# Kernel optimization log

Measured on AMD Instinct MI355X. Metric: run time of the kernel, lower is better.

Reference implementation:

```python
import jax, jax.numpy as jnp
import numpy as np


def setup_inputs() -> dict:
    key = jax.random.key(0)
    ks = jax.random.split(key, 6)
    C, C8, W, H, B = 512, 64, 64, 64, 4
    x = jax.random.normal(ks[0], (B, C, W, H), dtype=jnp.float32)
    Wf = jax.random.normal(ks[1], (C8, C), dtype=jnp.float32) * (1.0 / np.sqrt(C))
    Wg = jax.random.normal(ks[2], (C8, C), dtype=jnp.float32) * (1.0 / np.sqrt(C))
    Wh = jax.random.normal(ks[3], (C8, C), dtype=jnp.float32) * (1.0 / np.sqrt(C))
    Wv = jax.random.normal(ks[4], (C, C8), dtype=jnp.float32) * (1.0 / np.sqrt(C8))
    gamma = jax.random.normal(ks[5], (1,), dtype=jnp.float32)
    return {"x": x, "Wf": Wf, "Wg": Wg, "Wh": Wh, "Wv": Wv, "gamma": gamma}


def reference(x, Wf, Wg, Wh, Wv, gamma):
    b, c, w, h = x.shape
    n = w * h
    xf = x.reshape(b, c, n)                       # [b, c, n]
    # 1x1 convs == channel-mixing GEMMs
    f = jnp.einsum('oc,bcn->bon', Wf, xf)         # [b, c8, n]
    g = jnp.einsum('oc,bcn->bon', Wg, xf)         # [b, c8, n]
    hmap = jnp.einsum('oc,bcn->bon', Wh, xf)      # [b, c8, n]
    # attn_map[b, i, j] = sum_c f[b, c, i] * g[b, c, j]  (f permuted as in torch)
    attn = jnp.einsum('bci,bcj->bij', f, g)       # [b, n, n]
    # unconventional softmax over dim=1 (rows / the i axis)
    attn = jax.nn.softmax(attn, axis=1)
    sa = jnp.einsum('bcn,bnj->bcj', hmap, attn)   # [b, c8, n]
    sa = sa.reshape(b, -1, w, h)                  # [b, c8, w, h]
    sa = jnp.einsum('oc,bcwh->bowh', Wv, sa)      # [b, c, w, h]
    out = sa * gamma[0] + x
    return out, sa
```

## Files before the change

### kernel.cpp

```cpp
#include <hip/hip_runtime.h>
#include <cstddef>

#define BB 4
#define CC 512
#define NN 4096

using half8  = __attribute__((ext_vector_type(8))) _Float16;
using fp16x2 = __attribute__((ext_vector_type(2))) __fp16;
using short8 = __attribute__((ext_vector_type(8))) short;
using us8    = __attribute__((ext_vector_type(8))) unsigned short;
using f32x4  = __attribute__((ext_vector_type(4))) float;
using f32x16 = __attribute__((ext_vector_type(16))) float;

__device__ __forceinline__ unsigned short f2bf(float x) {
    unsigned int u = __float_as_uint(x);
    u += 0x7fffu + ((u >> 16) & 1u);
    return (unsigned short)(u >> 16);
}

__global__ __launch_bounds__(256) void prep_kernel(
    const float* __restrict__ Wf, const float* __restrict__ Wg,
    const float* __restrict__ Wh, const float* __restrict__ Wv,
    _Float16* __restrict__ Wc16, _Float16* __restrict__ Wv16)
{
    int idx = blockIdx.x * 256 + threadIdx.x;
    int stride = gridDim.x * 256;
    const int N1 = 192 * 512, N2 = 512 * 64;
    for (int i = idx; i < N1 + N2; i += stride) {
        if (i < N1) {
            int row = i >> 9, c = i & 511;
            const float* src = (row < 64) ? Wf : ((row < 128) ? Wg : Wh);
            float sc = (row >= 64 && row < 128) ? 1.4426950408889634f : 1.0f;
            Wc16[i] = (_Float16)(sc * src[(row & 63) * 512 + c]);
        } else {
            int k = i - N1;
            Wv16[k] = (_Float16)Wv[k];
        }
    }
}

__global__ __launch_bounds__(256) void proj_kernel(
    const float* __restrict__ x, const _Float16* __restrict__ Wc16,
    _Float16* __restrict__ Kf, _Float16* __restrict__ Qf,
    unsigned short* __restrict__ Vt)
{
    __shared__ float xsT[2][32][68];
    const int t    = threadIdx.x;
    const int w    = t >> 6;
    const int lane = t & 63;
    const int lh   = lane & 15;
    const int qd   = lane >> 4;
    const int b    = blockIdx.x >> 7;
    const int i0   = (blockIdx.x & 127) << 5;

    f32x4 acc[3][2];
    #pragma unroll
    for (int ot = 0; ot < 3; ot++)
        #pragma unroll
        for (int it = 0; it < 2; it++) { acc[ot][it][0]=0.f; acc[ot][it][1]=0.f; acc[ot][it][2]=0.f; acc[ot][it][3]=0.f; }

    const int ti8 = t & 7;
    const int tc2 = t >> 3;
    const float* xbase = x + (size_t)b*CC*NN + i0 + ti8*4;
    const _Float16* wbase = Wc16 + (size_t)(w*48 + lh)*512 + qd*8;

    float4 st0, st1;
    half8  wcur[2][3], wnxt[2][3];

#define LOADX(ck) do {                                                        \
    st0 = *(const float4*)(xbase + (size_t)((ck)*64 + tc2)*NN);               \
    st1 = *(const float4*)(xbase + (size_t)((ck)*64 + 32 + tc2)*NN);          \
} while (0)
#define STOREX(p_) do {                                                       \
    xsT[p_][ti8*4+0][tc2]    = st0.x; xsT[p_][ti8*4+1][tc2]    = st0.y;       \
    xsT[p_][ti8*4+2][tc2]    = st0.z; xsT[p_][ti8*4+3][tc2]    = st0.w;       \
    xsT[p_][ti8*4+0][32+tc2] = st1.x; xsT[p_][ti8*4+1][32+tc2] = st1.y;       \
    xsT[p_][ti8*4+2][32+tc2] = st1.z; xsT[p_][ti8*4+3][32+tc2] = st1.w;       \
} while (0)
#define LOADW(ck, WD) do {                                                    \
    _Pragma("unroll")                                                         \
    for (int ks_ = 0; ks_ < 2; ks_++)                                         \
        _Pragma("unroll")                                                     \
        for (int ot_ = 0; ot_ < 3; ot_++)                                     \
            WD[ks_][ot_] = *(const half8*)(wbase + (size_t)(ot_*16)*512 + (ck)*64 + ks_*32); \
} while (0)

    LOADX(0); STOREX(0);
    LOADW(0, wcur);
    __syncthreads();

    #pragma unroll
    for (int ck = 0; ck < 8; ck++) {
        const int p = ck & 1;
        if (ck < 7) { LOADX(ck + 1); LOADW(ck + 1, wnxt); }

        #pragma unroll
        for (int ks = 0; ks < 2; ks++) {
            half8 xf[2];
            #pragma unroll
            for (int it = 0; it < 2; it++) {
                const float* xr = &xsT[p][it*16 + lh][ks*32 + qd*8];
                f32x4 xa = *(const f32x4*)xr;
                f32x4 xb = *(const f32x4*)(xr + 4);
                union { fp16x2 h2[4]; half8 h8; } u;
                u.h2[0] = __builtin_amdgcn_cvt_pkrtz(xa[0], xa[1]);
                u.h2[1] = __builtin_amdgcn_cvt_pkrtz(xa[2], xa[3]);
                u.h2[2] = __builtin_amdgcn_cvt_pkrtz(xb[0], xb[1]);
                u.h2[3] = __builtin_amdgcn_cvt_pkrtz(xb[2], xb[3]);
                xf[it] = u.h8;
            }
            #pragma unroll
            for (int ot = 0; ot < 3; ot++)
                #pragma unroll
                for (int it = 0; it < 2; it++)
                    acc[ot][it] = __builtin_amdgcn_mfma_f32_16x16x32_f16(wcur[ks][ot], xf[it], acc[ot][it], 0, 0, 0);
        }

        if (ck < 7) {
            STOREX(p ^ 1);
            #pragma unroll
            for (int ks_ = 0; ks_ < 2; ks_++)
                #pragma unroll
                for (int ot_ = 0; ot_ < 3; ot_++)
                    wcur[ks_][ot_] = wnxt[ks_][ot_];
        }
        __syncthreads();
    }
#undef LOADX
#undef STOREX
#undef LOADW

    #pragma unroll
    for (int ot = 0; ot < 3; ot++) {
        int g16 = w*3 + ot;
        int m   = g16 >> 2;
        int obase = (g16 & 3)*16 + qd*4;
        #pragma unroll
        for (int it = 0; it < 2; it++) {
            int ig = i0 + it*16 + lh;
            #pragma unroll
            for (int r = 0; r < 4; r++) {
                float v = acc[ot][it][r];
                int ol = obase + r;
                if (m == 0)       Kf[((size_t)b*NN + ig)*64 + ol] = (_Float16)v;
                else if (m == 1)  Qf[((size_t)b*NN + ig)*64 + ol] = (_Float16)v;
                else              Vt[((size_t)b*64 + ol)*NN + ig] = f2bf(v);
            }
        }
    }
}

template<int SPLITS>
__global__ __launch_bounds__(256, 4) void attn_kernel(
    const _Float16* __restrict__ Kf, const _Float16* __restrict__ Qf,
    const unsigned short* __restrict__ Vt,
    _Float16* __restrict__ Po16, float* __restrict__ Pl)
{
    static_assert(NN % SPLITS == 0, "split");
    constexpr int KS  = NN / SPLITS;
    constexpr int NCH = KS / 64;

    __shared__ __align__(16) unsigned short Kb2[2][64*64];
    __shared__ __align__(16) unsigned short Vb2[2][64*64];

    const int t    = threadIdx.x;
    const int wv   = t >> 6;
    const int lane = t & 63;
    const int il   = lane & 31;
    const int h    = lane >> 5;

    const int p  = blockIdx.x;
    const int v  = (p & 7) * (SPLITS * 16) + (p >> 3);
    const int jt = v & 31;
    const int bs = v >> 5;
    const int b  = bs / SPLITS;
    const int s  = bs % SPLITS;
    const int j0w  = jt*128 + wv*32;
    const int koff = s * KS;

    half8 qfr[4];
    {
        const _Float16* qp = Qf + ((size_t)b*NN + j0w + il)*64 + h*8;
        #pragma unroll
        for (int sl = 0; sl < 4; sl++) qfr[sl] = *(const half8*)(qp + sl*16);
    }

    f32x16 o_acc[2];
    #pragma unroll
    for (int dt = 0; dt < 2; dt++)
        #pragma unroll
        for (int r = 0; r < 16; r++) o_acc[dt][r] = 0.f;
    float l4[4] = {0.f, 0.f, 0.f, 0.f};

    const int slot0 = t, slot1 = 256 + t;
    const int ik0 = slot0 >> 3, sw0 = ((slot0 & 7) ^ (ik0 & 7)) << 3;
    const int ik1 = slot1 >> 3, sw1 = ((slot1 & 7) ^ (ik1 & 7)) << 3;
    const _Float16*       gk0 = Kf + ((size_t)b*NN + koff + ik0)*64 + sw0;
    const _Float16*       gk1 = Kf + ((size_t)b*NN + koff + ik1)*64 + sw1;
    const unsigned short* gv0 = Vt + ((size_t)b*64 + ik0)*NN + koff + sw0;
    const unsigned short* gv1 = Vt + ((size_t)b*64 + ik1)*NN + koff + sw1;

#define STAGE(ck, pb) do {                                                          \
    const size_t o64_ = (size_t)(ck)*64;                                            \
    __builtin_amdgcn_global_load_lds(                                               \
        (const __attribute__((address_space(1))) void*)(gk0 + o64_*64),             \
        (__attribute__((address_space(3))) void*)&Kb2[pb][(wv*64)*8], 16, 0, 0);    \
    __builtin_amdgcn_global_load_lds(                                               \
        (const __attribute__((address_space(1))) void*)(gk1 + o64_*64),             \
        (__attribute__((address_space(3))) void*)&Kb2[pb][(256 + wv*64)*8], 16, 0, 0); \
    __builtin_amdgcn_global_load_lds(                                               \
        (const __attribute__((address_space(1))) void*)(gv0 + o64_),                \
        (__attribute__((address_space(3))) void*)&Vb2[pb][(wv*64)*8], 16, 0, 0);    \
    __builtin_amdgcn_global_load_lds(                                               \
        (const __attribute__((address_space(1))) void*)(gv1 + o64_),                \
        (__attribute__((address_space(3))) void*)&Vb2[pb][(256 + wv*64)*8], 16, 0, 0); \
    } while (0)

    STAGE(0, 0);
    __syncthreads();

    for (int ck = 0; ck < NCH; ck++) {
        const int cb = ck & 1;
        if (ck + 1 < NCH) STAGE(ck + 1, cb ^ 1);

        const unsigned short* Kb = Kb2[cb];
        const unsigned short* Vb = Vb2[cb];

        #pragma unroll
        for (int isub = 0; isub < 2; isub++) {
            const int irow = isub*32 + il;
            const unsigned short* kr = Kb + irow*64;
            f32x16 sc;
            #pragma unroll
            for (int r = 0; r < 16; r++) sc[r] = 0.f;
            __builtin_amdgcn_s_setprio(1);
            #pragma unroll
            for (int sl = 0; sl < 4; sl++) {
                half8 kf = *(const half8*)(kr + (((sl*2 + h) ^ (irow & 7)) << 3));
                sc = __builtin_amdgcn_mfma_f32_32x32x16_f16(kf, qfr[sl], sc, 0, 0, 0);
            }
            __builtin_amdgcn_s_setprio(0);

            #pragma unroll
            for (int r = 0; r < 16; r++) sc[r] = exp2f(sc[r]);
            #pragma unroll
            for (int r = 0; r < 16; r++) l4[r & 3] += sc[r];

            unsigned wA[8];
            #pragma unroll
            for (int k = 0; k < 8; k++)
                asm("v_cvt_pk_bf16_f32 %0, %1, %2" : "=v"(wA[k]) : "v"(sc[2*k]), "v"(sc[2*k+1]));
            asm("v_permlane32_swap_b32 %0, %1" : "+v"(wA[0]), "+v"(wA[2]));
            asm("v_permlane32_swap_b32 %0, %1" : "+v"(wA[1]), "+v"(wA[3]));
            asm("v_permlane32_swap_b32 %0, %1" : "+v"(wA[4]), "+v"(wA[6]));
            asm("v_permlane32_swap_b32 %0, %1" : "+v"(wA[5]), "+v"(wA[7]));

            union { unsigned u[4]; short8 s8; } pa0, pa1;
            pa0.u[0]=wA[0]; pa0.u[1]=wA[1]; pa0.u[2]=wA[2]; pa0.u[3]=wA[3];
            pa1.u[0]=wA[4]; pa1.u[1]=wA[5]; pa1.u[2]=wA[6]; pa1.u[3]=wA[7];

            __builtin_amdgcn_s_setprio(1);
            #pragma unroll
            for (int isl = 0; isl < 2; isl++) {
                const short8 paf = isl ? pa1.s8 : pa0.s8;
                const int vc = isub*4 + isl*2 + h;
                #pragma unroll
                for (int dt = 0; dt < 2; dt++) {
                    const int drow = dt*32 + il;
                    short8 vf = *(const short8*)(Vb + drow*64 + ((vc ^ (drow & 7)) << 3));
                    o_acc[dt] = __builtin_amdgcn_mfma_f32_32x32x16_bf16(paf, vf, o_acc[dt], 0, 0, 0);
                }
            }
            __builtin_amdgcn_s_setprio(0);
        }
        __syncthreads();
    }
#undef STAGE

    float l_acc  = (l4[0] + l4[1]) + (l4[2] + l4[3]);
    float l_full = l_acc + __shfl_xor(l_acc, 32);
    float inv = 1.0f / l_full;

    const size_t pbase = (size_t)(s*4 + b)*NN + j0w;
    #pragma unroll
    for (int r = 0; r < 16; r++) {
        const int jr = (r & 3) + 8*(r >> 2) + 4*h;
        const float invr = __shfl(inv, jr);
        #pragma unroll
        for (int dt = 0; dt < 2; dt++)
            Po16[(pbase + jr)*64 + dt*32 + il] = (_Float16)(o_acc[dt][r] * invr);
    }
    if (h == 0) Pl[pbase + il] = l_full;
}

template<int SPLITS>
__global__ __launch_bounds__(256) void outproj_kernel(
    const _Float16* __restrict__ Po16, const float* __restrict__ Pl,
    const _Float16* __restrict__ Wv16,
    const float* __restrict__ x, const float* __restrict__ gamma,
    float* __restrict__ out1, float* __restrict__ out2)
{
    __shared__ float Osh[4][16][36];
    const int t    = threadIdx.x;
    const int w    = t >> 6;
    const int lane = t & 63;
    const int lh   = lane & 15;
    const int qd   = lane >> 4;
    const int b    = blockIdx.x >> 7;
    const int j0   = (blockIdx.x & 127) << 5;
    const float g  = gamma[0];

    half8 sb[2][2];
    #pragma unroll
    for (int jt2 = 0; jt2 < 2; jt2++) {
        const int j = j0 + jt2*16 + lh;
        float os[16];
        #pragma unroll
        for (int k = 0; k < 16; k++) os[k] = 0.f;
        float lsum = 0.f;
        #pragma unroll
        for (int s = 0; s < SPLITS; s++) {
            size_t base = ((size_t)(s*4 + b)*NN + j);
            half8 v0 = *(const half8*)(Po16 + base*64 + qd*8);
            half8 v1 = *(const half8*)(Po16 + base*64 + qd*8 + 32);
            float l = Pl[base];
            #pragma unroll
            for (int k = 0; k < 8; k++) {
                os[k]   = fmaf(l, (float)v0[k], os[k]);
                os[8+k] = fmaf(l, (float)v1[k], os[8+k]);
            }
            lsum += l;
        }
        float inv = 1.0f / lsum;
        union { fp16x2 h2[4]; half8 h8; } u0, u1;
        #pragma unroll
        for (int k = 0; k < 4; k++) {
            u0.h2[k] = __builtin_amdgcn_cvt_pkrtz(os[2*k]*inv,   os[2*k+1]*inv);
            u1.h2[k] = __builtin_amdgcn_cvt_pkrtz(os[8+2*k]*inv, os[8+2*k+1]*inv);
        }
        sb[jt2][0] = u0.h8;
        sb[jt2][1] = u1.h8;
    }

    const int o_loc8 = lane >> 3;
    const int j4     = (lane & 7) * 4;

    #pragma unroll 2
    for (int ot8 = 0; ot8 < 8; ot8++) {
        const int ot = w*8 + ot8;
        const size_t wbase = (size_t)(ot*16 + lh)*64 + qd*8;
        half8 a0 = *(const half8*)(Wv16 + wbase);
        half8 a1 = *(const half8*)(Wv16 + wbase + 32);

        f32x4 acc[2];
        #pragma unroll
        for (int jt2 = 0; jt2 < 2; jt2++) {
            acc[jt2][0]=0.f; acc[jt2][1]=0.f; acc[jt2][2]=0.f; acc[jt2][3]=0.f;
            acc[jt2] = __builtin_amdgcn_mfma_f32_16x16x32_f16(a0, sb[jt2][0], acc[jt2], 0, 0, 0);
            acc[jt2] = __builtin_amdgcn_mfma_f32_16x16x32_f16(a1, sb[jt2][1], acc[jt2], 0, 0, 0);
        }

        #pragma unroll
        for (int jt2 = 0; jt2 < 2; jt2++)
            #pragma unroll
            for (int r = 0; r < 4; r++)
                Osh[w][qd*4 + r][jt2*16 + lh] = acc[jt2][r];
        asm volatile("s_waitcnt lgkmcnt(0)" ::: "memory");

        #pragma unroll
        for (int rr2 = 0; rr2 < 2; rr2++) {
            const int o_loc = o_loc8 + 8*rr2;
            f32x4 v = *(const f32x4*)&Osh[w][o_loc][j4];
            const int o  = ot*16 + o_loc;
            const size_t idx = ((size_t)b*CC + o)*NN + j0 + j4;
            f32x4 xv = *(const f32x4*)(x + idx);
            *(f32x4*)(out2 + idx) = v;
            f32x4 r1;
            r1[0] = fmaf(g, v[0], xv[0]); r1[1] = fmaf(g, v[1], xv[1]);
            r1[2] = fmaf(g, v[2], xv[2]); r1[3] = fmaf(g, v[3], xv[3]);
            *(f32x4*)(out1 + idx) = r1;
        }
        asm volatile("s_waitcnt lgkmcnt(0)" ::: "memory");
    }
}

extern "C" void kernel_launch(void* const* d_in, const int* in_sizes, int n_in,
                              void* d_out, int out_size, void* d_ws, size_t ws_size,
                              hipStream_t stream) {
    const float* x     = (const float*)d_in[0];
    const float* Wf    = (const float*)d_in[1];
    const float* Wg    = (const float*)d_in[2];
    const float* Wh    = (const float*)d_in[3];
    const float* Wv    = (const float*)d_in[4];
    const float* gamma = (const float*)d_in[5];

    float* out1 = (float*)d_out;
    float* out2 = out1 + (size_t)BB*CC*NN;

    const size_t BND = (size_t)BB*NN*64;
    const size_t need8 = BND*2*3 + BND*2*8 + (size_t)8*BB*NN*4
                       + (size_t)192*512*2 + (size_t)512*64*2;
    const int SPL = (ws_size >= need8) ? 8 : 4;

    char* wp = (char*)d_ws;
    _Float16*       Kf   = (_Float16*)wp;        wp += BND*2;
    _Float16*       Qf   = (_Float16*)wp;        wp += BND*2;
    unsigned short* Vt   = (unsigned short*)wp;  wp += BND*2;
    _Float16*       Po16 = (_Float16*)wp;        wp += BND*2*SPL;
    float*          Pl   = (float*)wp;           wp += (size_t)SPL*BB*NN*4;
    _Float16*       Wc16 = (_Float16*)wp;        wp += (size_t)192*512*2;
    _Float16*       Wv16 = (_Float16*)wp;

    prep_kernel<<<dim3(64), dim3(256), 0, stream>>>(Wf, Wg, Wh, Wv, Wc16, Wv16);
    proj_kernel<<<dim3(BB*128), dim3(256), 0, stream>>>(x, Wc16, Kf, Qf, Vt);
    if (SPL == 8) {
        attn_kernel<8><<<dim3(128*8), dim3(256), 0, stream>>>(Kf, Qf, Vt, Po16, Pl);
        outproj_kernel<8><<<dim3(512), dim3(256), 0, stream>>>(Po16, Pl, Wv16, x, gamma, out1, out2);
    } else {
        attn_kernel<4><<<dim3(128*4), dim3(256), 0, stream>>>(Kf, Qf, Vt, Po16, Pl);
        outproj_kernel<4><<<dim3(512), dim3(256), 0, stream>>>(Po16, Pl, Wv16, x, gamma, out1, out2);
    }
}
```

Before: 165.3 us.

## Triple-buffer attention K/V staging and halve outproj tile width

The attention kernel moves from double to triple buffered LDS staging, prefetching two chunks ahead and waiting with partial vmcnt counts plus raw s_barrier in place of a full __syncthreads per chunk. This is meant to hide global-to-LDS latency, at the cost of more LDS per block and a lower occupancy hint (3 blocks instead of 4). Separately, outproj now processes 16 columns per block instead of 32 and launches twice as many blocks, aiming for more parallelism in the memory-bound epilogue. Each outproj block now does a single MFMA tile per output group, so reuse of the Wv16 weights is lower.

```diff
diff --git a/kernel.cpp b/kernel.cpp
--- a/kernel.cpp
+++ b/kernel.cpp
@@ -151,7 +151,7 @@
 }
 
 template<int SPLITS>
-__global__ __launch_bounds__(256, 4) void attn_kernel(
+__global__ __launch_bounds__(256, 3) void attn_kernel(
     const _Float16* __restrict__ Kf, const _Float16* __restrict__ Qf,
     const unsigned short* __restrict__ Vt,
     _Float16* __restrict__ Po16, float* __restrict__ Pl)
@@ -159,9 +159,10 @@
     static_assert(NN % SPLITS == 0, "split");
     constexpr int KS  = NN / SPLITS;
     constexpr int NCH = KS / 64;
-
-    __shared__ __align__(16) unsigned short Kb2[2][64*64];
-    __shared__ __align__(16) unsigned short Vb2[2][64*64];
+    static_assert(NCH >= 3, "need >=3 chunks for 3-buffer pipeline");
+
+    __shared__ __align__(16) unsigned short Kb2[3][64*64];
+    __shared__ __align__(16) unsigned short Vb2[3][64*64];
 
     const int t    = threadIdx.x;
     const int wv   = t >> 6;
@@ -217,11 +218,15 @@
     } while (0)
 
     STAGE(0, 0);
-    __syncthreads();
-
+    STAGE(1, 1);
+    asm volatile("s_waitcnt vmcnt(4)" ::: "memory");
+    __builtin_amdgcn_sched_barrier(0);
+    __builtin_amdgcn_s_barrier();
+    __builtin_amdgcn_sched_barrier(0);
+
+    int cb = 0, nb = 2;
     for (int ck = 0; ck < NCH; ck++) {
-        const int cb = ck & 1;
-        if (ck + 1 < NCH) STAGE(ck + 1, cb ^ 1);
+        if (ck + 2 < NCH) STAGE(ck + 2, nb);
 
         const unsigned short* Kb = Kb2[cb];
         const unsigned short* Vb = Vb2[cb];
@@ -273,7 +278,17 @@
             }
             __builtin_amdgcn_s_setprio(0);
         }
-        __syncthreads();
+
+        if (ck + 1 < NCH) {
+            if (ck + 2 < NCH) asm volatile("s_waitcnt vmcnt(4)" ::: "memory");
+            else              asm volatile("s_waitcnt vmcnt(0)" ::: "memory");
+            __builtin_amdgcn_sched_barrier(0);
+            __builtin_amdgcn_s_barrier();
+            __builtin_amdgcn_sched_barrier(0);
+        }
+
+        cb = (cb == 2) ? 0 : cb + 1;
+        nb = (nb == 2) ? 0 : nb + 1;
     }
 #undef STAGE
 
@@ -300,20 +315,19 @@
     const float* __restrict__ x, const float* __restrict__ gamma,
     float* __restrict__ out1, float* __restrict__ out2)
 {
-    __shared__ float Osh[4][16][36];
+    __shared__ float Osh[4][16][20];
     const int t    = threadIdx.x;
     const int w    = t >> 6;
     const int lane = t & 63;
     const int lh   = lane & 15;
     const int qd   = lane >> 4;
-    const int b    = blockIdx.x >> 7;
-    const int j0   = (blockIdx.x & 127) << 5;
+    const int b    = blockIdx.x >> 8;
+    const int j0   = (blockIdx.x & 255) << 4;
     const float g  = gamma[0];
 
-    half8 sb[2][2];
-    #pragma unroll
-    for (int jt2 = 0; jt2 < 2; jt2++) {
-        const int j = j0 + jt2*16 + lh;
+    half8 sb0, sb1;
+    {
+        const int j = j0 + lh;
         float os[16];
         #pragma unroll
         for (int k = 0; k < 16; k++) os[k] = 0.f;
@@ -338,12 +352,12 @@
             u0.h2[k] = __builtin_amdgcn_cvt_pkrtz(os[2*k]*inv,   os[2*k+1]*inv);
             u1.h2[k] = __builtin_amdgcn_cvt_pkrtz(os[8+2*k]*inv, os[8+2*k+1]*inv);
         }
-        sb[jt2][0] = u0.h8;
-        sb[jt2][1] = u1.h8;
-    }
-
-    const int o_loc8 = lane >> 3;
-    const int j4     = (lane & 7) * 4;
+        sb0 = u0.h8;
+        sb1 = u1.h8;
+    }
+
+    const int o_loc = lane >> 2;
+    const int j4    = (lane & 3) * 4;
 
     #pragma unroll 2
     for (int ot8 = 0; ot8 < 8; ot8++) {
@@ -352,34 +366,25 @@
         half8 a0 = *(const half8*)(Wv16 + wbase);
         half8 a1 = *(const half8*)(Wv16 + wbase + 32);
 
-        f32x4 acc[2];
-        #pragma unroll
-        for (int jt2 = 0; jt2 < 2; jt2++) {
-            acc[jt2][0]=0.f; acc[jt2][1]=0.f; acc[jt2][2]=0.f; acc[jt2][3]=0.f;
-            acc[jt2] = __builtin_amdgcn_mfma_f32_16x16x32_f16(a0, sb[jt2][0], acc[jt2], 0, 0, 0);
-            acc[jt2] = __builtin_amdgcn_mfma_f32_16x16x32_f16(a1, sb[jt2][1], acc[jt2], 0, 0, 0);
-        }
-
-        #pragma unroll
-        for (int jt2 = 0; jt2 < 2; jt2++)
-            #pragma unroll
-            for (int r = 0; r < 4; r++)
-                Osh[w][qd*4 + r][jt2*16 + lh] = acc[jt2][r];
+        f32x4 acc;
+        acc[0]=0.f; acc[1]=0.f; acc[2]=0.f; acc[3]=0.f;
+        acc = __builtin_amdgcn_mfma_f32_16x16x32_f16(a0, sb0, acc, 0, 0, 0);
+        acc = __builtin_amdgcn_mfma_f32_16x16x32_f16(a1, sb1, acc, 0, 0, 0);
+
+        #pragma unroll
+        for (int r = 0; r < 4; r++)
+            Osh[w][qd*4 + r][lh] = acc[r];
         asm volatile("s_waitcnt lgkmcnt(0)" ::: "memory");
 
-        #pragma unroll
-        for (int rr2 = 0; rr2 < 2; rr2++) {
-            const int o_loc = o_loc8 + 8*rr2;
-            f32x4 v = *(const f32x4*)&Osh[w][o_loc][j4];
-            const int o  = ot*16 + o_loc;
-            const size_t idx = ((size_t)b*CC + o)*NN + j0 + j4;
-            f32x4 xv = *(const f32x4*)(x + idx);
-            *(f32x4*)(out2 + idx) = v;
-            f32x4 r1;
-            r1[0] = fmaf(g, v[0], xv[0]); r1[1] = fmaf(g, v[1], xv[1]);
-            r1[2] = fmaf(g, v[2], xv[2]); r1[3] = fmaf(g, v[3], xv[3]);
-            *(f32x4*)(out1 + idx) = r1;
-        }
+        f32x4 vv = *(const f32x4*)&Osh[w][o_loc][j4];
+        const int o  = ot*16 + o_loc;
+        const size_t idx = ((size_t)b*CC + o)*NN + j0 + j4;
+        f32x4 xv = *(const f32x4*)(x + idx);
+        *(f32x4*)(out2 + idx) = vv;
+        f32x4 r1;
+        r1[0] = fmaf(g, vv[0], xv[0]); r1[1] = fmaf(g, vv[1], xv[1]);
+        r1[2] = fmaf(g, vv[2], xv[2]); r1[3] = fmaf(g, vv[3], xv[3]);
+        *(f32x4*)(out1 + idx) = r1;
         asm volatile("s_waitcnt lgkmcnt(0)" ::: "memory");
     }
 }
@@ -415,9 +420,9 @@
     proj_kernel<<<dim3(BB*128), dim3(256), 0, stream>>>(x, Wc16, Kf, Qf, Vt);
     if (SPL == 8) {
         attn_kernel<8><<<dim3(128*8), dim3(256), 0, stream>>>(Kf, Qf, Vt, Po16, Pl);
-        outproj_kernel<8><<<dim3(512), dim3(256), 0, stream>>>(Po16, Pl, Wv16, x, gamma, out1, out2);
+        outproj_kernel<8><<<dim3(BB*256), dim3(256), 0, stream>>>(Po16, Pl, Wv16, x, gamma, out1, out2);
     } else {
         attn_kernel<4><<<dim3(128*4), dim3(256), 0, stream>>>(Kf, Qf, Vt, Po16, Pl);
-        outproj_kernel<4><<<dim3(512), dim3(256), 0, stream>>>(Po16, Pl, Wv16, x, gamma, out1, out2);
-    }
-}
+        outproj_kernel<4><<<dim3(BB*256), dim3(256), 0, stream>>>(Po16, Pl, Wv16, x, gamma, out1, out2);
+    }
+}
```

Result: slower. 170.4 us (+3.1%).
